# Kernel optimization log

Hardware: AMD Instinct MI355X
Metric: run time of the kernel (lower is better)

The kernel has to match this reference:

```python
import jax, jax.numpy as jnp
import numpy as np

NUM_EXPERTS = 8
TOP_K = 2


def setup_inputs() -> dict:
    key = jax.random.key(0)
    k1, k2, k3, k4, k5 = jax.random.split(key, 5)
    B, S, H, I, E = 2, 2048, 1024, 3584, NUM_EXPERTS
    scale_h = 1.0 / np.sqrt(H)
    scale_i = 1.0 / np.sqrt(I)
    return {
        "hidden_states": jax.random.normal(k1, (B, S, H), dtype=jnp.float32),
        "gate_w": jax.random.normal(k2, (H, E), dtype=jnp.float32) * scale_h,
        "w1": jax.random.normal(k3, (E, H, I), dtype=jnp.float32) * scale_h,
        "w3": jax.random.normal(k4, (E, H, I), dtype=jnp.float32) * scale_h,
        "w2": jax.random.normal(k5, (E, I, H), dtype=jnp.float32) * scale_i,
    }


def reference(hidden_states, gate_w, w1, w3, w2):
    # Router: [B,S,H] @ [H,E] -> [B,S,E]
    router_logits = jnp.einsum("bsh,he->bse", hidden_states, gate_w).astype(jnp.float32)
    routing_weights, selected_experts = jax.lax.top_k(router_logits, k=TOP_K)
    routing_weights = jax.nn.softmax(routing_weights, axis=-1)  # [B,S,TOP_K]

    final_hidden_state = jnp.zeros_like(hidden_states)
    # Dense loop over all experts (faithful to the original mask-multiply-accumulate)
    for index in range(NUM_EXPERTS):
        h1 = jax.nn.silu(jnp.einsum("bsh,hi->bsi", hidden_states, w1[index]))
        h3 = jnp.einsum("bsh,hi->bsi", hidden_states, w3[index])
        expert_out = jnp.einsum("bsi,ih->bsh", h1 * h3, w2[index])
        # Per-token routing weight for this expert (0 if not selected)
        weight = jnp.sum(
            jnp.where(selected_experts == index, routing_weights, 0.0), axis=-1
        )[:, :, None]  # [B,S,1]
        final_hidden_state = final_hidden_state + weight * expert_out
    return final_hidden_state, router_logits
```

## Files before the change

### kernel.cpp

```cpp
#include <hip/hip_runtime.h>


typedef __bf16 v8bf  __attribute__((ext_vector_type(8)));
typedef float  v16f  __attribute__((ext_vector_type(16)));

constexpr int kT = 4096;
constexpr int kH = 1024;
constexpr int kI = 3584;
constexpr int kE = 8;

constexpr size_t SZ_W    = (size_t)kE * kI * kH * 2;
constexpr size_t OFF_W1T = 0;
constexpr size_t OFF_W3T = OFF_W1T + SZ_W;
constexpr size_t OFF_W2T = OFF_W3T + SZ_W;
constexpr size_t OFF_XG  = OFF_W2T + SZ_W;
constexpr size_t OFF_ACT = OFF_XG  + (size_t)2*kT*kH*2;
constexpr size_t OFF_BUF = OFF_W1T;
constexpr size_t OFF_CNT = OFF_ACT + (size_t)2*kT*kI*2;
constexpr size_t OFF_OFS = OFF_CNT + 128;
constexpr size_t OFF_LST = OFF_OFS + 128;
constexpr size_t OFF_TW  = OFF_LST + (size_t)kE*kT*4;
constexpr size_t OFF_TR  = OFF_TW  + (size_t)kT*2*4;

__device__ __forceinline__ void async16(void* lds, const void* g) {
    __builtin_amdgcn_global_load_lds(
        (const __attribute__((address_space(1))) unsigned int*)g,
        (__attribute__((address_space(3))) unsigned int*)lds,
        16, 0, 0);
}

__global__ void zero_counts_kernel(int* __restrict__ counts) {
    if (threadIdx.x < kE) counts[threadIdx.x] = 0;
}

__global__ void prefix_kernel(const int* __restrict__ counts, int* __restrict__ offsets) {
    if (threadIdx.x == 0) {
        int o = 0;
        for (int e = 0; e < kE; e++) { offsets[e] = o; o += counts[e]; }
    }
}

__global__ void router_kernel(const float* __restrict__ x, const float* __restrict__ gw,
                              float* __restrict__ logits_out, float* __restrict__ tw,
                              int* __restrict__ counts, int* __restrict__ list) {
    const int wave = threadIdx.x >> 6;
    const int lane = threadIdx.x & 63;
    const int t = blockIdx.x * 4 + wave;
    const float* xr = x + (size_t)t * kH;

    double acc[kE];
#pragma unroll
    for (int e = 0; e < kE; e++) acc[e] = 0.0;

    for (int j = 0; j < kH / 64; j++) {
        const int h = j * 64 + lane;
        const float xv = xr[h];
        const float* g = gw + (size_t)h * kE;
#pragma unroll
        for (int e = 0; e < kE; e++) acc[e] += (double)xv * (double)g[e];
    }
#pragma unroll
    for (int e = 0; e < kE; e++) {
#pragma unroll
        for (int o = 32; o > 0; o >>= 1) acc[e] += __shfl_xor(acc[e], o, 64);
    }

    if (lane == 0) {
        float lg[kE];
#pragma unroll
        for (int e = 0; e < kE; e++) lg[e] = (float)acc[e];
#pragma unroll
        for (int e = 0; e < kE; e++) logits_out[(size_t)t * kE + e] = lg[e];

        int e0 = 0; float l0 = lg[0];
        for (int e = 1; e < kE; e++) if (lg[e] > l0) { l0 = lg[e]; e0 = e; }
        int e1 = -1; float l1 = -3.4e38f;
        for (int e = 0; e < kE; e++) if (e != e0 && lg[e] > l1) { l1 = lg[e]; e1 = e; }

        const float ex = __expf(l1 - l0);
        const float w0 = 1.0f / (1.0f + ex);
        const float w1 = ex / (1.0f + ex);

        int s0 = atomicAdd(&counts[e0], 1);
        list[e0 * kT + s0] = t * 2 + 0;
        tw[t * 2 + 0] = w0;
        int s1 = atomicAdd(&counts[e1], 1);
        list[e1 * kT + s1] = t * 2 + 1;
        tw[t * 2 + 1] = w1;
    }
}

__global__ void gather_kernel(const float* __restrict__ x, const int* __restrict__ list,
                              const int* __restrict__ counts, const int* __restrict__ offsets,
                              __bf16* __restrict__ xg, int* __restrict__ trow) {
    const int g = blockIdx.x;
    int e = 0;
    while (e < kE - 1 && g >= offsets[e] + counts[e]) e++;
    const int s = g - offsets[e];
    const int entry = list[e * kT + s];
    const int t = entry >> 1;
    if (threadIdx.x == 0) trow[entry] = g;
    const int i = threadIdx.x * 4;
    const float4 v = *(const float4*)&x[(size_t)t * kH + i];
    __bf16 pk[4] = {(__bf16)v.x, (__bf16)v.y, (__bf16)v.z, (__bf16)v.w};
    *(ushort4*)&xg[(size_t)g * kH + i] = *(const ushort4*)pk;
}

__global__ void transpose_cvt_all_kernel(const float* __restrict__ w1, const float* __restrict__ w3,
                                         const float* __restrict__ w2,
                                         __bf16* __restrict__ w1t, __bf16* __restrict__ w3t,
                                         __bf16* __restrict__ w2t) {
    __shared__ float tile[64][65];
    const int z = blockIdx.z;
    const float* s; __bf16* d; int R, C;
    if (z < 8)       { s = w1 + (size_t)z * kH * kI;        d = w1t + (size_t)z * kH * kI;        R = kH; C = kI; }
    else if (z < 16) { s = w3 + (size_t)(z - 8) * kH * kI;  d = w3t + (size_t)(z - 8) * kH * kI;  R = kH; C = kI; }
    else             { s = w2 + (size_t)(z - 16) * kI * kH; d = w2t + (size_t)(z - 16) * kI * kH; R = kI; C = kH; }
    const int ntx = C / 64;
    const int tx = blockIdx.x % ntx, ty = blockIdx.x / ntx;
    const int r0 = ty * 64, c0 = tx * 64;
    const int tr = threadIdx.x >> 4;
    const int tc = (threadIdx.x & 15) * 4;
#pragma unroll
    for (int i = 0; i < 4; i++) {
        const float4 v = *(const float4*)&s[(size_t)(r0 + tr + i * 16) * C + (c0 + tc)];
        tile[tr + i * 16][tc + 0] = v.x;
        tile[tr + i * 16][tc + 1] = v.y;
        tile[tr + i * 16][tc + 2] = v.z;
        tile[tr + i * 16][tc + 3] = v.w;
    }
    __syncthreads();
#pragma unroll
    for (int i = 0; i < 4; i++) {
        const int oc = tr + i * 16;
        __bf16 pk[4] = {(__bf16)tile[tc + 0][oc], (__bf16)tile[tc + 1][oc],
                        (__bf16)tile[tc + 2][oc], (__bf16)tile[tc + 3][oc]};
        *(ushort4*)&d[(size_t)(c0 + oc) * R + r0 + tc] = *(const ushort4*)pk;
    }
}

__global__ __launch_bounds__(256, 2) void gemm1_kernel(
    const __bf16* __restrict__ xg, const __bf16* __restrict__ w1t,
    const __bf16* __restrict__ w3t, __bf16* __restrict__ act,
    const int* __restrict__ counts, const int* __restrict__ offsets) {
    const int e = blockIdx.z;
    const int cnt = counts[e];
    const int m0 = blockIdx.y * 128;
    if (m0 >= cnt) return;
    const int n0 = blockIdx.x * 128;
    const int off = offsets[e];

    __shared__ __bf16 As[128 * 32], B1s[128 * 32], B3s[128 * 32];

    const int tid = threadIdx.x;
    const int lane = tid & 63, wave = tid >> 6;
    const int wm = (wave >> 1) * 64, wn = (wave & 1) * 64;
    const int l31 = lane & 31;
    const int half = lane >> 5;

    const int scol = ((tid & 3) ^ ((tid >> 2) & 3)) * 8;
    const __bf16* abase[2];
    const __bf16* b1base[2];
    const __bf16* b3base[2];
    const __bf16* w1b = w1t + (size_t)e * kI * kH + (size_t)n0 * kH;
    const __bf16* w3b = w3t + (size_t)e * kI * kH + (size_t)n0 * kH;
#pragma unroll
    for (int p = 0; p < 2; p++) {
        const int r = p * 64 + (tid >> 2);
        const int gr = min(m0 + r, cnt - 1);
        abase[p]  = xg + (size_t)(off + gr) * kH + scol;
        b1base[p] = w1b + (size_t)r * kH + scol;
        b3base[p] = w3b + (size_t)r * kH + scol;
    }

    const int ph0 = (half ^ (lane & 3)) * 8;
    const int ph1 = ((half ^ 2) ^ (lane & 3)) * 8;

    v16f acc1[2][2], acc3[2][2];
#pragma unroll
    for (int i = 0; i < 2; i++)
#pragma unroll
        for (int j = 0; j < 2; j++) { acc1[i][j] = (v16f)0.0f; acc3[i][j] = (v16f)0.0f; }

    for (int kt = 0; kt < kH / 32; kt++) {
        const int k0 = kt * 32;
#pragma unroll
        for (int p = 0; p < 2; p++) {
            const int soff = p * 2048 + tid * 8;
            async16(&As[soff],  abase[p]  + k0);
            async16(&B1s[soff], b1base[p] + k0);
            async16(&B3s[soff], b3base[p] + k0);
        }
        __syncthreads();

#pragma unroll
        for (int ks = 0; ks < 2; ks++) {
            const int ph = ks ? ph1 : ph0;
            v8bf a[2], b1[2], b3[2];
#pragma unroll
            for (int f = 0; f < 2; f++) {
                a[f]  = *(const v8bf*)&As [(wm + f * 32 + l31) * 32 + ph];
                b1[f] = *(const v8bf*)&B1s[(wn + f * 32 + l31) * 32 + ph];
                b3[f] = *(const v8bf*)&B3s[(wn + f * 32 + l31) * 32 + ph];
            }
#pragma unroll
            for (int fn = 0; fn < 2; fn++)
#pragma unroll
                for (int fm = 0; fm < 2; fm++) {
                    acc1[fm][fn] = __builtin_amdgcn_mfma_f32_32x32x16_bf16(a[fm], b1[fn], acc1[fm][fn], 0, 0, 0);
                    acc3[fm][fn] = __builtin_amdgcn_mfma_f32_32x32x16_bf16(a[fm], b3[fn], acc3[fm][fn], 0, 0, 0);
                }
        }
        __syncthreads();
    }

#pragma unroll
    for (int fm = 0; fm < 2; fm++) {
#pragma unroll
        for (int fn = 0; fn < 2; fn++) {
            const v16f c1 = acc1[fm][fn], c3 = acc3[fm][fn];
            const int col = n0 + wn + fn * 32 + l31;
#pragma unroll
            for (int reg = 0; reg < 16; reg++) {
                const int rloc = (reg & 3) + 8 * (reg >> 2) + 4 * half;
                const int gm = m0 + wm + fm * 32 + rloc;
                if (gm < cnt) {
                    const float h1 = c1[reg], h3 = c3[reg];
                    const float v = h1 / (1.0f + __expf(-h1)) * h3;
                    act[(size_t)(off + gm) * kI + col] = (__bf16)v;
                }
            }
        }
    }
}

__global__ __launch_bounds__(256, 2) void gemm2_kernel(
    const __bf16* __restrict__ act, const __bf16* __restrict__ w2t,
    float* __restrict__ buf,
    const int* __restrict__ counts, const int* __restrict__ offsets) {
    const int e = blockIdx.z;
    const int cnt = counts[e];
    const int m0 = blockIdx.y * 128;
    if (m0 >= cnt) return;
    const int n0 = blockIdx.x * 128;
    const int off = offsets[e];

    __shared__ __bf16 As[128 * 32], Bs[128 * 32];

    const int tid = threadIdx.x;
    const int lane = tid & 63, wave = tid >> 6;
    const int wm = (wave >> 1) * 64, wn = (wave & 1) * 64;
    const int l31 = lane & 31;
    const int half = lane >> 5;

    const int scol = ((tid & 3) ^ ((tid >> 2) & 3)) * 8;
    const __bf16* abase[2];
    const __bf16* bbase[2];
    const __bf16* w2b = w2t + (size_t)e * kH * kI + (size_t)n0 * kI;
#pragma unroll
    for (int p = 0; p < 2; p++) {
        const int r = p * 64 + (tid >> 2);
        const int gr = min(m0 + r, cnt - 1);
        abase[p] = act + (size_t)(off + gr) * kI + scol;
        bbase[p] = w2b + (size_t)r * kI + scol;
    }

    const int ph0 = (half ^ (lane & 3)) * 8;
    const int ph1 = ((half ^ 2) ^ (lane & 3)) * 8;

    v16f acc[2][2];
#pragma unroll
    for (int i = 0; i < 2; i++)
#pragma unroll
        for (int j = 0; j < 2; j++) acc[i][j] = (v16f)0.0f;

    for (int kt = 0; kt < kI / 32; kt++) {
        const int k0 = kt * 32;
#pragma unroll
        for (int p = 0; p < 2; p++) {
            const int soff = p * 2048 + tid * 8;
            async16(&As[soff], abase[p] + k0);
            async16(&Bs[soff], bbase[p] + k0);
        }
        __syncthreads();

#pragma unroll
        for (int ks = 0; ks < 2; ks++) {
            const int ph = ks ? ph1 : ph0;
            v8bf a[2], b[2];
#pragma unroll
            for (int f = 0; f < 2; f++) {
                a[f] = *(const v8bf*)&As[(wm + f * 32 + l31) * 32 + ph];
                b[f] = *(const v8bf*)&Bs[(wn + f * 32 + l31) * 32 + ph];
            }
#pragma unroll
            for (int fn = 0; fn < 2; fn++)
#pragma unroll
                for (int fm = 0; fm < 2; fm++)
                    acc[fm][fn] = __builtin_amdgcn_mfma_f32_32x32x16_bf16(a[fm], b[fn], acc[fm][fn], 0, 0, 0);
        }
        __syncthreads();
    }

#pragma unroll
    for (int fm = 0; fm < 2; fm++) {
#pragma unroll
        for (int fn = 0; fn < 2; fn++) {
            const v16f c = acc[fm][fn];
            const int col = n0 + wn + fn * 32 + l31;
#pragma unroll
            for (int reg = 0; reg < 16; reg++) {
                const int rloc = (reg & 3) + 8 * (reg >> 2) + 4 * half;
                const int gm = m0 + wm + fm * 32 + rloc;
                if (gm < cnt) buf[(size_t)(off + gm) * kH + col] = c[reg];
            }
        }
    }
}

__global__ void combine_kernel(const float* __restrict__ buf, const int* __restrict__ trow,
                               const float* __restrict__ tw, float* __restrict__ out) {
    const int t = blockIdx.x;
    const int r0 = trow[2 * t], r1 = trow[2 * t + 1];
    const float w0 = tw[2 * t], w1 = tw[2 * t + 1];
    const int i = threadIdx.x * 4;
    const float4 a = *(const float4*)&buf[(size_t)r0 * kH + i];
    const float4 b = *(const float4*)&buf[(size_t)r1 * kH + i];
    float4 o;
    o.x = w0 * a.x + w1 * b.x;
    o.y = w0 * a.y + w1 * b.y;
    o.z = w0 * a.z + w1 * b.z;
    o.w = w0 * a.w + w1 * b.w;
    *(float4*)&out[(size_t)t * kH + i] = o;
}

extern "C" void kernel_launch(void* const* d_in, const int* in_sizes, int n_in,
                              void* d_out, int out_size, void* d_ws, size_t ws_size,
                              hipStream_t stream) {
    const float* x  = (const float*)d_in[0];
    const float* gw = (const float*)d_in[1];
    const float* w1 = (const float*)d_in[2];
    const float* w3 = (const float*)d_in[3];
    const float* w2 = (const float*)d_in[4];
    float* out = (float*)d_out;
    float* logits_out = out + (size_t)kT * kH;

    char* ws = (char*)d_ws;
    __bf16* w1t   = (__bf16*)(ws + OFF_W1T);
    __bf16* w3t   = (__bf16*)(ws + OFF_W3T);
    __bf16* w2t   = (__bf16*)(ws + OFF_W2T);
    __bf16* xg    = (__bf16*)(ws + OFF_XG);
    __bf16* act   = (__bf16*)(ws + OFF_ACT);
    float*  buf   = (float*) (ws + OFF_BUF);
    int*    cnt   = (int*)   (ws + OFF_CNT);
    int*    ofs   = (int*)   (ws + OFF_OFS);
    int*    list  = (int*)   (ws + OFF_LST);
    float*  tw    = (float*) (ws + OFF_TW);
    int*    trow  = (int*)   (ws + OFF_TR);

    zero_counts_kernel<<<1, 64, 0, stream>>>(cnt);

    transpose_cvt_all_kernel<<<dim3(896, 1, 24), 256, 0, stream>>>(w1, w3, w2, w1t, w3t, w2t);

    router_kernel<<<kT / 4, 256, 0, stream>>>(x, gw, logits_out, tw, cnt, list);
    prefix_kernel<<<1, 1, 0, stream>>>(cnt, ofs);
    gather_kernel<<<2 * kT, 256, 0, stream>>>(x, list, cnt, ofs, xg, trow);

    gemm1_kernel<<<dim3(kI / 128, kT / 128, kE), 256, 0, stream>>>(xg, w1t, w3t, act, cnt, ofs);
    gemm2_kernel<<<dim3(kH / 128, kT / 128, kE), 256, 0, stream>>>(act, w2t, buf, cnt, ofs);

    combine_kernel<<<kT, 256, 0, stream>>>(buf, trow, tw, out);
}
```

Baseline: 816.4 us.

## Fuse weighted combine into gemm2 epilogue via atomics and retune LDS swizzle

Removes the combine kernel and the fp32 intermediate buffer. gemm2 now scales each output row by its routing weight and atomically adds it into the zeroed output, using per-row token and weight tables written by the gather kernel. The LDS XOR swizzle pattern is also changed for both GEMMs, aiming to reduce bank conflicts. The atomics add contention and make the summation order nondeterministic, and the output now needs a memset.

Result: no change. 817.2 us (+0.1%).

```diff
diff --git a/kernel.cpp b/kernel.cpp
--- a/kernel.cpp
+++ b/kernel.cpp
@@ -15,12 +15,12 @@
 constexpr size_t OFF_W2T = OFF_W3T + SZ_W;
 constexpr size_t OFF_XG  = OFF_W2T + SZ_W;
 constexpr size_t OFF_ACT = OFF_XG  + (size_t)2*kT*kH*2;
-constexpr size_t OFF_BUF = OFF_W1T;
 constexpr size_t OFF_CNT = OFF_ACT + (size_t)2*kT*kI*2;
 constexpr size_t OFF_OFS = OFF_CNT + 128;
 constexpr size_t OFF_LST = OFF_OFS + 128;
 constexpr size_t OFF_TW  = OFF_LST + (size_t)kE*kT*4;
-constexpr size_t OFF_TR  = OFF_TW  + (size_t)kT*2*4;
+constexpr size_t OFF_RT  = OFF_TW  + (size_t)kT*2*4;
+constexpr size_t OFF_RW  = OFF_RT  + (size_t)2*kT*4;
 
 __device__ __forceinline__ void async16(void* lds, const void* g) {
     __builtin_amdgcn_global_load_lds(
@@ -92,14 +92,16 @@
 
 __global__ void gather_kernel(const float* __restrict__ x, const int* __restrict__ list,
                               const int* __restrict__ counts, const int* __restrict__ offsets,
-                              __bf16* __restrict__ xg, int* __restrict__ trow) {
+                              const float* __restrict__ tw,
+                              __bf16* __restrict__ xg, int* __restrict__ rowt,
+                              float* __restrict__ roww) {
     const int g = blockIdx.x;
     int e = 0;
     while (e < kE - 1 && g >= offsets[e] + counts[e]) e++;
     const int s = g - offsets[e];
     const int entry = list[e * kT + s];
     const int t = entry >> 1;
-    if (threadIdx.x == 0) trow[entry] = g;
+    if (threadIdx.x == 0) { rowt[g] = t; roww[g] = tw[entry]; }
     const int i = threadIdx.x * 4;
     const float4 v = *(const float4*)&x[(size_t)t * kH + i];
     __bf16 pk[4] = {(__bf16)v.x, (__bf16)v.y, (__bf16)v.z, (__bf16)v.w};
@@ -158,7 +160,7 @@
     const int l31 = lane & 31;
     const int half = lane >> 5;
 
-    const int scol = ((tid & 3) ^ ((tid >> 2) & 3)) * 8;
+    const int scol = ((tid & 3) ^ ((tid >> 3) & 3)) * 8;
     const __bf16* abase[2];
     const __bf16* b1base[2];
     const __bf16* b3base[2];
@@ -173,8 +175,9 @@
         b3base[p] = w3b + (size_t)r * kH + scol;
     }
 
-    const int ph0 = (half ^ (lane & 3)) * 8;
-    const int ph1 = ((half ^ 2) ^ (lane & 3)) * 8;
+    const int rsw = (l31 >> 1) & 3;
+    const int ph0 = (half ^ rsw) * 8;
+    const int ph1 = ((half ^ 2) ^ rsw) * 8;
 
     v16f acc1[2][2], acc3[2][2];
 #pragma unroll
@@ -236,8 +239,9 @@
 
 __global__ __launch_bounds__(256, 2) void gemm2_kernel(
     const __bf16* __restrict__ act, const __bf16* __restrict__ w2t,
-    float* __restrict__ buf,
-    const int* __restrict__ counts, const int* __restrict__ offsets) {
+    float* __restrict__ out,
+    const int* __restrict__ counts, const int* __restrict__ offsets,
+    const int* __restrict__ rowt, const float* __restrict__ roww) {
     const int e = blockIdx.z;
     const int cnt = counts[e];
     const int m0 = blockIdx.y * 128;
@@ -253,7 +257,7 @@
     const int l31 = lane & 31;
     const int half = lane >> 5;
 
-    const int scol = ((tid & 3) ^ ((tid >> 2) & 3)) * 8;
+    const int scol = ((tid & 3) ^ ((tid >> 3) & 3)) * 8;
     const __bf16* abase[2];
     const __bf16* bbase[2];
     const __bf16* w2b = w2t + (size_t)e * kH * kI + (size_t)n0 * kI;
@@ -265,8 +269,9 @@
         bbase[p] = w2b + (size_t)r * kI + scol;
     }
 
-    const int ph0 = (half ^ (lane & 3)) * 8;
-    const int ph1 = ((half ^ 2) ^ (lane & 3)) * 8;
+    const int rsw = (l31 >> 1) & 3;
+    const int ph0 = (half ^ rsw) * 8;
+    const int ph1 = ((half ^ 2) ^ rsw) * 8;
 
     v16f acc[2][2];
 #pragma unroll
@@ -312,26 +317,15 @@
             for (int reg = 0; reg < 16; reg++) {
                 const int rloc = (reg & 3) + 8 * (reg >> 2) + 4 * half;
                 const int gm = m0 + wm + fm * 32 + rloc;
-                if (gm < cnt) buf[(size_t)(off + gm) * kH + col] = c[reg];
+                if (gm < cnt) {
+                    const int row = off + gm;
+                    const int t = rowt[row];
+                    const float w = roww[row];
+                    atomicAdd(&out[(size_t)t * kH + col], w * c[reg]);
+                }
             }
         }
     }
-}
-
-__global__ void combine_kernel(const float* __restrict__ buf, const int* __restrict__ trow,
-                               const float* __restrict__ tw, float* __restrict__ out) {
-    const int t = blockIdx.x;
-    const int r0 = trow[2 * t], r1 = trow[2 * t + 1];
-    const float w0 = tw[2 * t], w1 = tw[2 * t + 1];
-    const int i = threadIdx.x * 4;
-    const float4 a = *(const float4*)&buf[(size_t)r0 * kH + i];
-    const float4 b = *(const float4*)&buf[(size_t)r1 * kH + i];
-    float4 o;
-    o.x = w0 * a.x + w1 * b.x;
-    o.y = w0 * a.y + w1 * b.y;
-    o.z = w0 * a.z + w1 * b.z;
-    o.w = w0 * a.w + w1 * b.w;
-    *(float4*)&out[(size_t)t * kH + i] = o;
 }
 
 extern "C" void kernel_launch(void* const* d_in, const int* in_sizes, int n_in,
@@ -351,23 +345,22 @@
     __bf16* w2t   = (__bf16*)(ws + OFF_W2T);
     __bf16* xg    = (__bf16*)(ws + OFF_XG);
     __bf16* act   = (__bf16*)(ws + OFF_ACT);
-    float*  buf   = (float*) (ws + OFF_BUF);
     int*    cnt   = (int*)   (ws + OFF_CNT);
     int*    ofs   = (int*)   (ws + OFF_OFS);
     int*    list  = (int*)   (ws + OFF_LST);
     float*  tw    = (float*) (ws + OFF_TW);
-    int*    trow  = (int*)   (ws + OFF_TR);
-
+    int*    rowt  = (int*)   (ws + OFF_RT);
+    float*  roww  = (float*) (ws + OFF_RW);
+
+    hipMemsetAsync(out, 0, (size_t)kT * kH * sizeof(float), stream);
     zero_counts_kernel<<<1, 64, 0, stream>>>(cnt);
 
     transpose_cvt_all_kernel<<<dim3(896, 1, 24), 256, 0, stream>>>(w1, w3, w2, w1t, w3t, w2t);
 
     router_kernel<<<kT / 4, 256, 0, stream>>>(x, gw, logits_out, tw, cnt, list);
     prefix_kernel<<<1, 1, 0, stream>>>(cnt, ofs);
-    gather_kernel<<<2 * kT, 256, 0, stream>>>(x, list, cnt, ofs, xg, trow);
+    gather_kernel<<<2 * kT, 256, 0, stream>>>(x, list, cnt, ofs, tw, xg, rowt, roww);
 
     gemm1_kernel<<<dim3(kI / 128, kT / 128, kE), 256, 0, stream>>>(xg, w1t, w3t, act, cnt, ofs);
-    gemm2_kernel<<<dim3(kH / 128, kT / 128, kE), 256, 0, stream>>>(act, w2t, buf, cnt, ofs);
-
-    combine_kernel<<<kT, 256, 0, stream>>>(buf, trow, tw, out);
-}
+    gemm2_kernel<<<dim3(kH / 128, kT / 128, kE), 256, 0, stream>>>(act, w2t, out, cnt, ofs, rowt, roww);
+}
```
